# Kernel tuning notes

Hardware: AMD Instinct MI355X
Metric: run time of the kernel (lower is better)

The kernel has to match this reference:

```python
import jax, jax.numpy as jnp
import numpy as np

B, D, Q, E, H, V = 32, 1024, 64, 384, 384, 50000
PAD = 0
EPS = 1e-12


def setup_inputs() -> dict:
    key = jax.random.key(0)
    ks = jax.random.split(key, 13)
    documents = jax.random.randint(ks[0], (B, D), 1, V)
    doc_lens = jax.random.randint(ks[1], (B,), D // 2, D + 1)
    doc_valid = jnp.arange(D)[None, :] < doc_lens[:, None]
    documents = jnp.where(doc_valid, documents, PAD)
    doc_masks = doc_valid.astype(jnp.float32)[:, :, None]
    querys = jax.random.randint(ks[2], (B, Q), 1, V)
    query_lens = jax.random.randint(ks[3], (B,), Q // 2, Q + 1)
    q_valid = jnp.arange(Q)[None, :] < query_lens[:, None]
    querys = jnp.where(q_valid, querys, PAD)
    query_masks = q_valid.astype(jnp.float32)[:, :, None]
    answers = documents[:, :1]  # guaranteed present in each doc
    emb = jax.random.uniform(ks[4], (V + 1, E), jnp.float32, -0.05, 0.05)
    emb = emb.at[PAD].set(0.0)
    gw = lambda k, s: jax.random.normal(k, s, jnp.float32) * 0.05
    w_ih_f = gw(ks[5], (3 * H, E)); w_hh_f = gw(ks[6], (3 * H, H))
    b_ih_f = gw(ks[7], (3 * H,)); b_hh_f = gw(ks[8], (3 * H,))
    w_ih_b = gw(ks[9], (3 * H, E)); w_hh_b = gw(ks[10], (3 * H, H))
    b_ih_b = gw(ks[11], (3 * H,)); b_hh_b = gw(ks[12], (3 * H,))
    return dict(documents=documents, doc_lens=doc_lens, doc_masks=doc_masks,
                querys=querys, query_lens=query_lens, query_masks=query_masks,
                answers=answers, emb=emb,
                w_ih_f=w_ih_f, w_hh_f=w_hh_f, b_ih_f=b_ih_f, b_hh_f=b_hh_f,
                w_ih_b=w_ih_b, w_hh_b=w_hh_b, b_ih_b=b_ih_b, b_hh_b=b_hh_b)


def _gru_dir(x, w_ih, w_hh, b_ih, b_hh):
    # x: [B,T,E] -> outputs [B,T,H]; torch GRU cell math
    Bn = x.shape[0]
    Hn = w_hh.shape[1]
    xp = jnp.einsum('bte,ge->btg', x, w_ih) + b_ih  # precompute input projections [B,T,3H]

    def step(h, g):
        gh = h @ w_hh.T + b_hh
        i_r, i_z, i_n = jnp.split(g, 3, axis=-1)
        h_r, h_z, h_n = jnp.split(gh, 3, axis=-1)
        r = jax.nn.sigmoid(i_r + h_r)
        z = jax.nn.sigmoid(i_z + h_z)
        n = jnp.tanh(i_n + r * h_n)
        hn = (1.0 - z) * n + z * h
        return hn, hn

    h0 = jnp.zeros((Bn, Hn), x.dtype)
    _, out = jax.lax.scan(step, h0, jnp.swapaxes(xp, 0, 1))
    return jnp.swapaxes(out, 0, 1)


def _rev_within_len(x, lens):
    # reverse each sequence only over its valid prefix (emulates packed bwd GRU)
    T = x.shape[1]
    t = jnp.arange(T)
    idx = jnp.where(t[None, :] < lens[:, None], lens[:, None] - 1 - t[None, :], t[None, :])
    return jnp.take_along_axis(x, idx[:, :, None], axis=1)


def _bigru(x, lens, valid, pf, pb):
    out_f = _gru_dir(x, *pf)
    out_b = _rev_within_len(_gru_dir(_rev_within_len(x, lens), *pb), lens)
    out = jnp.concatenate([out_f, out_b], axis=-1)
    return out * valid[:, :, None]  # unpack pads with zeros


def _softmax_mask(x, mask, axis):
    shift = jnp.max(x, axis=axis, keepdims=True)
    e = jnp.exp(x - shift) * mask
    return e / (jnp.sum(e, axis=axis, keepdims=True) + EPS)


def reference(documents, doc_lens, doc_masks, querys, query_lens, query_masks, answers,
              emb, w_ih_f, w_hh_f, b_ih_f, b_hh_f, w_ih_b, w_hh_b, b_ih_b, b_hh_b):
    doc_valid = doc_masks[..., 0]
    q_valid = query_masks[..., 0]
    doc_h = _bigru(emb[documents], doc_lens, doc_valid,
                   (w_ih_f, w_hh_f, b_ih_f, b_hh_f), (w_ih_b, w_hh_b, b_ih_b, b_hh_b))
    q_h = _bigru(emb[querys], query_lens, q_valid,
                 (w_ih_f, w_hh_f, b_ih_f, b_hh_f), (w_ih_b, w_hh_b, b_ih_b, b_hh_b))
    scores = jnp.einsum('bdh,bqh->bdq', doc_h, q_h)          # IndiATT_output
    pair_mask = jnp.einsum('bdo,bqo->bdq', doc_masks, query_masks)
    alpha = _softmax_mask(scores, pair_mask, axis=1)
    beta = _softmax_mask(scores, pair_mask, axis=2)
    beta_aver = jnp.sum(beta, axis=1) / doc_lens[:, None].astype(scores.dtype)  # [B,Q]
    s = jnp.einsum('bdq,bq->bd', alpha, beta_aver)            # AoA_output squeezed
    probs = jnp.sum(s * (documents == answers).astype(s.dtype), axis=1)

    def pick(doc, sv, vv):
        sc = jnp.zeros(V + 1, s.dtype).at[doc].add(sv * vv)   # segment-sum by word id
        cnt = jnp.zeros(V + 1, s.dtype).at[doc].add(vv)
        return jnp.argmax(jnp.where(cnt > 0, sc, -jnp.inf))

    pred_answers = jax.vmap(pick)(documents, s, doc_valid)
    return probs, pred_answers
```

## Files before the change

kernel.cpp:

```cpp
#include <hip/hip_runtime.h>
#include <hip/hip_bf16.h>
#include <stdint.h>

#define EPSV 1e-12f
#define NB 32
#define DD 1024
#define QQ 64
#define EE 384
#define HH 384
#define NW 12
#define CH 256

typedef __attribute__((ext_vector_type(4))) float f32x4;
typedef __attribute__((ext_vector_type(8))) __bf16 bf16x8;
typedef __attribute__((ext_vector_type(4))) unsigned short u16x4;
typedef __attribute__((ext_vector_type(4))) int i32x4;
typedef unsigned short u16;

static __device__ __forceinline__ u16 f2bf(float f) {
  union { float f; uint32_t u; } v; v.f = f;
  uint32_t u = v.u;
  return (u16)((u + 0x7fffu + ((u >> 16) & 1u)) >> 16);
}

static __device__ __forceinline__ f32x4 MFMA(bf16x8 a, bf16x8 b, f32x4 c) {
  return __builtin_amdgcn_mfma_f32_16x16x32_bf16(a, b, c, 0, 0, 0);
}

static __device__ __forceinline__ bf16x8 ldw8(const float* p) {
  float4 a = *(const float4*)p;
  float4 b = *(const float4*)(p + 4);
  union { u16 e[8]; bf16x8 v; } u;
  u.e[0] = f2bf(a.x); u.e[1] = f2bf(a.y); u.e[2] = f2bf(a.z); u.e[3] = f2bf(a.w);
  u.e[4] = f2bf(b.x); u.e[5] = f2bf(b.y); u.e[6] = f2bf(b.z); u.e[7] = f2bf(b.w);
  return u.v;
}

static __device__ __forceinline__ void st_short_sc(u16* p, u16 v) {
  asm volatile("global_store_short %0, %1, off sc1" :: "v"(p), "v"((uint32_t)v) : "memory");
}
static __device__ __forceinline__ void ld_b128_sc(const u16* p, i32x4& d) {
  asm volatile("global_load_dwordx4 %0, %1, off sc1" : "=v"(d) : "v"(p) : "memory");
}
static __device__ __forceinline__ void st_dword_sc(unsigned* p, unsigned v) {
  asm volatile("global_store_dword %0, %1, off sc1" :: "v"(p), "v"(v) : "memory");
}
static __device__ __forceinline__ void ld_tags(const unsigned* p, i32x4& a, i32x4& b, i32x4& c,
                                               i32x4& d, i32x4& e, i32x4& f) {
  asm volatile(
      "global_load_dwordx4 %0, %6, off sc1\n\t"
      "global_load_dwordx4 %1, %6, off offset:16 sc1\n\t"
      "global_load_dwordx4 %2, %6, off offset:32 sc1\n\t"
      "global_load_dwordx4 %3, %6, off offset:48 sc1\n\t"
      "global_load_dwordx4 %4, %6, off offset:64 sc1\n\t"
      "global_load_dwordx4 %5, %6, off offset:80 sc1\n\t"
      "s_waitcnt vmcnt(0)"
      : "=&v"(a), "=&v"(b), "=&v"(c), "=&v"(d), "=&v"(e), "=&v"(f)
      : "v"(p) : "memory");
}

__global__ __launch_bounds__(256) void k_emb(const int* __restrict__ doc, const int* __restrict__ qry,
                                             const float* __restrict__ emb, u16* __restrict__ embx) {
  int i = blockIdx.x * 256 + threadIdx.x;
  int row = i / 96, e4 = i - row * 96;
  int tok = (row < NB * DD) ? doc[row] : qry[row - NB * DD];
  float4 v = ((const float4*)(emb + (size_t)tok * EE))[e4];
  u16x4 o; o.x = f2bf(v.x); o.y = f2bf(v.y); o.z = f2bf(v.z); o.w = f2bf(v.w);
  *(u16x4*)(embx + (size_t)row * EE + e4 * 4) = o;
}

__global__ __launch_bounds__(512, 2) void k_xp(
    const u16* __restrict__ embx, const int* __restrict__ doc_lens, const int* __restrict__ q_lens,
    const float* __restrict__ w_ih_f, const float* __restrict__ b_ih_f, const float* __restrict__ b_hh_f,
    const float* __restrict__ w_ih_b, const float* __restrict__ b_ih_b, const float* __restrict__ b_hh_b,
    float* __restrict__ xpd, float* __restrict__ xpq, int cbase) {
  __shared__ int lensh[32];
  const int gx = blockIdx.x;
  int corpus, d2, jblk, tch;
  if (gx < 48) { corpus = 0; d2 = gx / 24; int rem = gx % 24; jblk = rem / 4; tch = rem % 4; }
  else { corpus = 1; int g2 = gx - 48; d2 = g2 / 6; jblk = g2 % 6; tch = 0; }
  const int T = corpus ? QQ : DD;
  const int* lens = corpus ? q_lens : doc_lens;
  const float* w_ih = d2 ? w_ih_b : w_ih_f;
  const float* b_ih = d2 ? b_ih_b : b_ih_f;
  const float* b_hh = d2 ? b_hh_b : b_hh_f;
  const u16* exb = embx + (corpus ? (size_t)NB * DD * EE : 0);
  float* xpg = corpus ? (xpq + (size_t)d2 * QQ * 36864) : (xpd + (size_t)d2 * CH * 36864);
  const int tid = threadIdx.x;
  if (tid < 32) lensh[tid] = lens[tid];
  __syncthreads();
  const int lane = tid & 63, wv = tid >> 6;
  const int wslot = wv >> 1, mt = wv & 1;
  const int col = lane & 15, khi = lane >> 4;
  const int jg = jblk * 64 + wslot * 16 + col;
  const float br = b_ih[jg] + b_hh[jg];
  const float bz = b_ih[384 + jg] + b_hh[384 + jg];
  const float bn = b_ih[768 + jg];
  bf16x8 Wr[12], Wz[12], Wn[12];
#pragma unroll
  for (int ks = 0; ks < 12; ++ks) {
    Wr[ks] = ldw8(w_ih + (size_t)jg * 384 + ks * 32 + khi * 8);
    Wz[ks] = ldw8(w_ih + (size_t)(384 + jg) * 384 + ks * 32 + khi * 8);
    Wn[ks] = ldw8(w_ih + (size_t)(768 + jg) * 384 + ks * 32 + khi * 8);
  }
  const int b_a = mt * 16 + col;
  const int lenb = lensh[b_a];
  const int bh0 = mt * 16 + khi * 4;
  for (int tt = 0; tt < 64; ++tt) {
    const int s_lc = tch * 64 + tt;
    const int s_g = corpus ? s_lc : (cbase + s_lc);
    const int trow = d2 ? ((s_g < lenb) ? (lenb - 1 - s_g) : s_g) : s_g;
    const u16* ap = exb + ((size_t)b_a * T + trow) * EE + khi * 8;
    bf16x8 A[12];
#pragma unroll
    for (int ks = 0; ks < 12; ++ks) A[ks] = *(const bf16x8*)(ap + ks * 32);
    f32x4 ar{0.f, 0.f, 0.f, 0.f}, az = ar, an = ar;
#pragma unroll
    for (int ks = 0; ks < 12; ++ks) {
      ar = MFMA(A[ks], Wr[ks], ar);
      az = MFMA(A[ks], Wz[ks], az);
      an = MFMA(A[ks], Wn[ks], an);
    }
    float* op = xpg + (size_t)s_lc * 36864 + (size_t)jg * 32 + bh0;
    f32x4 o0{ar[0] + br, ar[1] + br, ar[2] + br, ar[3] + br};
    f32x4 o1{az[0] + bz, az[1] + bz, az[2] + bz, az[3] + bz};
    f32x4 o2{an[0] + bn, an[1] + bn, an[2] + bn, an[3] + bn};
    *(f32x4*)op = o0;
    *(f32x4*)(op + 384 * 32) = o1;
    *(f32x4*)(op + 768 * 32) = o2;
  }
}

__global__ __launch_bounds__(256) void k_rec(
    const float* __restrict__ xpd, const float* __restrict__ xpq,
    const int* __restrict__ doc_lens, const int* __restrict__ q_lens,
    const float* __restrict__ w_hh_f, const float* __restrict__ b_hh_f,
    const float* __restrict__ w_hh_b, const float* __restrict__ b_hh_b,
    u16* __restrict__ doc_h, u16* __restrict__ q_h,
    u16* __restrict__ h_bc, unsigned* __restrict__ cnts, unsigned* __restrict__ tags,
    float* __restrict__ h_state, int cbase, int first) {
  __shared__ u16 wfrag[36864];
  __shared__ int lensh[32];

  const int grp = blockIdx.x / NW;
  const int wg = blockIdx.x - grp * NW;
  const int corpus = grp >> 1, dir = grp & 1;
  const int T = corpus ? QQ : DD;
  const int nst = corpus ? QQ : CH;
  const int* lens = corpus ? q_lens : doc_lens;
  const float* w_hh = dir ? w_hh_b : w_hh_f;
  const float* b_hh = dir ? b_hh_b : b_hh_f;
  u16* out = corpus ? q_h : doc_h;
  const float* xpg = corpus ? (xpq + (size_t)dir * QQ * 36864) : (xpd + (size_t)dir * CH * 36864);
  u16* hb = h_bc + (size_t)grp * (2 * NB * HH);
  unsigned* cnt = cnts + (size_t)grp * 16;
  const int tid = threadIdx.x;

  if (tid < 32) lensh[tid] = lens[tid];
  for (int idx = tid; idx < 36864; idx += 256) {
    int nt = idx / 6144;
    int rem = idx - nt * 6144;
    int ks = rem >> 9;
    int le = rem & 511;
    int lane_ = le >> 3, i = le & 7;
    int g = nt >> 1, js_ = nt & 1;
    int colw = lane_ & 15, khiw = lane_ >> 4;
    int k = ks * 32 + khiw * 8 + i;
    int rowg = g * 384 + wg * 32 + js_ * 16 + colw;
    wfrag[idx] = f2bf(w_hh[(size_t)rowg * 384 + k]);
  }
  if (first) {
    for (int idx = tid; idx < 1024; idx += 256) {
      int b = idx >> 5, jl_ = idx & 31;
      st_short_sc(hb + b * HH + wg * 32 + jl_, (u16)0);
    }
    asm volatile("s_waitcnt vmcnt(0)" ::: "memory");
  }
  __syncthreads();
  if (first) {
    if (tid == 0) {
      __hip_atomic_fetch_add(cnt, 1u, __ATOMIC_RELAXED, __HIP_MEMORY_SCOPE_AGENT);
      while (__hip_atomic_load(cnt, __ATOMIC_RELAXED, __HIP_MEMORY_SCOPE_AGENT) < (unsigned)NW)
        __builtin_amdgcn_s_sleep(1);
    }
    __syncthreads();
  }

  const int lane = tid & 63, wv = tid >> 6;
  const int mt = wv >> 1, js = wv & 1;
  const int col = lane & 15, khi = lane >> 4;
  const int jg = wg * 32 + js * 16 + col;
  const float bias_hn = b_hh[768 + jg];
  const int b_x = mt * 16 + col;
  const int bh0 = mt * 16 + khi * 4;
  int len_h[4];
#pragma unroll
  for (int r = 0; r < 4; ++r) len_h[r] = lensh[bh0 + r];
  u16* outp = out + (size_t)dir * HH + jg;
  f32x4 hprev;
#pragma unroll
  for (int r = 0; r < 4; ++r)
    hprev[r] = first ? 0.f : h_state[(size_t)grp * 12288 + (size_t)jg * 32 + (bh0 + r)];

  const unsigned* tagrow = tags + (size_t)grp * 64 + mt * 32;
  unsigned* tagp = tags + (size_t)grp * 64 + mt * 32 + (wg * 2 + js);

  auto umin2 = [](unsigned a, unsigned b) { return a < b ? a : b; };
  auto pollwait = [&](unsigned need) {
    while (true) {
      i32x4 t0, t1, t2, t3, t4, t5;
      ld_tags(tagrow, t0, t1, t2, t3, t4, t5);
      unsigned mn = 0xffffffffu;
#pragma unroll
      for (int k = 0; k < 4; ++k) {
        mn = umin2(mn, (unsigned)t0[k]); mn = umin2(mn, (unsigned)t1[k]);
        mn = umin2(mn, (unsigned)t2[k]); mn = umin2(mn, (unsigned)t3[k]);
        mn = umin2(mn, (unsigned)t4[k]); mn = umin2(mn, (unsigned)t5[k]);
      }
      if (mn >= need) break;
      __builtin_amdgcn_s_sleep(1);
    }
  };
  auto load_xp = [&](f32x4* x, int sl) {
    const float* xs = xpg + (size_t)sl * 36864;
#pragma unroll
    for (int g = 0; g < 3; ++g)
      x[g] = *(const f32x4*)(xs + ((size_t)(g * 384 + jg)) * 32 + bh0);
  };

  f32x4 xpA[3], xpB[3];
  load_xp(xpA, 0);

  auto step = [&](int sl, f32x4* xc, f32x4* xn) {
    const int s = cbase + sl;
    const int p = s & 1;
    const u16* rbuf = hb + p * (NB * HH);
    u16* wbuf = hb + (p ^ 1) * (NB * HH);
    pollwait((unsigned)s);
    i32x4 areg[12];
    const u16* ahp = rbuf + b_x * HH + khi * 8;
#pragma unroll
    for (int ks = 0; ks < 12; ++ks) ld_b128_sc(ahp + ks * 32, areg[ks]);
    asm volatile("s_waitcnt vmcnt(0)" ::: "memory");
    __builtin_amdgcn_sched_barrier(0);
    f32x4 acc_r{0.f, 0.f, 0.f, 0.f};
    f32x4 acc_z = acc_r, acc_nh = acc_r;
#pragma unroll
    for (int ks = 0; ks < 12; ++ks) {
      bf16x8 af = __builtin_bit_cast(bf16x8, areg[ks]);
      bf16x8 br = *(const bf16x8*)&wfrag[((js) * 12 + ks) * 512 + lane * 8];
      bf16x8 bz = *(const bf16x8*)&wfrag[((2 + js) * 12 + ks) * 512 + lane * 8];
      bf16x8 bn = *(const bf16x8*)&wfrag[((4 + js) * 12 + ks) * 512 + lane * 8];
      acc_r = MFMA(af, br, acc_r);
      acc_z = MFMA(af, bz, acc_z);
      acc_nh = MFMA(af, bn, acc_nh);
    }
    u16 hq[4];
#pragma unroll
    for (int r = 0; r < 4; ++r) {
      const int b = bh0 + r;
      float rg = 1.f / (1.f + __expf(-(acc_r[r] + xc[0][r])));
      float zg = 1.f / (1.f + __expf(-(acc_z[r] + xc[1][r])));
      float ng = tanhf(xc[2][r] + rg * (acc_nh[r] + bias_hn));
      float hn = (1.f - zg) * ng + zg * hprev[r];
      hprev[r] = hn;
      hq[r] = f2bf(hn);
      st_short_sc(wbuf + b * HH + jg, hq[r]);
    }
    asm volatile("s_waitcnt vmcnt(0)" ::: "memory");
    if (lane == 0) st_dword_sc(tagp, (unsigned)(s + 1));
    load_xp(xn, (sl + 1 < nst) ? (sl + 1) : sl);
#pragma unroll
    for (int r = 0; r < 4; ++r) {
      const int b = bh0 + r;
      const int len = len_h[r];
      const int tro = dir ? ((s < len) ? (len - 1 - s) : s) : s;
      outp[((size_t)b * T + tro) * (2 * HH)] = hq[r];
    }
  };

  for (int sl = 0; sl < nst; sl += 2) {
    step(sl, xpA, xpB);
    step(sl + 1, xpB, xpA);
  }
#pragma unroll
  for (int r = 0; r < 4; ++r)
    h_state[(size_t)grp * 12288 + (size_t)jg * 32 + (bh0 + r)] = hprev[r];
}

__global__ __launch_bounds__(256) void k_scores(
    const u16* __restrict__ doc_h, const u16* __restrict__ q_h,
    const int* __restrict__ doc_lens, const int* __restrict__ q_lens,
    float* __restrict__ SM, float* __restrict__ rowmax, float* __restrict__ rowsum) {
  const int b = blockIdx.x >> 4, dblk = blockIdx.x & 15;
  const int tid = threadIdx.x, lane = tid & 63, wv = tid >> 6;
  const int col = lane & 15, khi = lane >> 4;
  const int dlen = doc_lens[b], qlen = q_lens[b];
  const u16* dp = doc_h + ((size_t)(b * DD + dblk * 64 + wv * 16 + col)) * (2 * HH) + khi * 8;
  const u16* qp = q_h + (size_t)b * QQ * (2 * HH);
  f32x4 acc[4];
#pragma unroll
  for (int nt = 0; nt < 4; ++nt) acc[nt] = f32x4{0.f, 0.f, 0.f, 0.f};
  for (int ks = 0; ks < 24; ++ks) {
    bf16x8 av = *(const bf16x8*)(dp + ks * 32);
#pragma unroll
    for (int nt = 0; nt < 4; ++nt) {
      bf16x8 bv = *(const bf16x8*)(qp + (size_t)(nt * 16 + col) * (2 * HH) + ks * 32 + khi * 8);
      acc[nt] = MFMA(av, bv, acc[nt]);
    }
  }
  const int d0 = dblk * 64 + wv * 16 + khi * 4;
  float* smb = SM + (size_t)b * DD * QQ;
#pragma unroll
  for (int r = 0; r < 4; ++r) {
    const int d = d0 + r;
    const bool dv = d < dlen;
    float v[4];
#pragma unroll
    for (int nt = 0; nt < 4; ++nt) {
      const int q = nt * 16 + col;
      v[nt] = (dv && q < qlen) ? acc[nt][r] : 0.f;
      smb[(size_t)d * QQ + q] = v[nt];
    }
    float mx = fmaxf(fmaxf(v[0], v[1]), fmaxf(v[2], v[3]));
#pragma unroll
    for (int off = 1; off < 16; off <<= 1) mx = fmaxf(mx, __shfl_xor(mx, off, 64));
    float sm = 0.f;
#pragma unroll
    for (int nt = 0; nt < 4; ++nt) {
      const int q = nt * 16 + col;
      if (dv && q < qlen) sm += __expf(v[nt] - mx);
    }
#pragma unroll
    for (int off = 1; off < 16; off <<= 1) sm += __shfl_xor(sm, off, 64);
    if (col == 0) { rowmax[b * DD + d] = mx; rowsum[b * DD + d] = sm; }
  }
}

__global__ __launch_bounds__(256) void k_cols(
    const float* __restrict__ SM, const float* __restrict__ rowmax, const float* __restrict__ rowsum,
    const int* __restrict__ doc_lens, const int* __restrict__ q_lens,
    float* __restrict__ colmax, float* __restrict__ colsum, float* __restrict__ bav) {
  const int b = blockIdx.x, tid = threadIdx.x;
  const int q = tid & 63, dg = tid >> 6;
  __shared__ float red[4][64];
  __shared__ float cmx[64];
  const float* smb = SM + (size_t)b * DD * QQ;
  float cm = -3.0e38f;
  for (int d = dg; d < DD; d += 4) cm = fmaxf(cm, smb[(size_t)d * QQ + q]);
  red[dg][q] = cm;
  __syncthreads();
  if (tid < 64) cmx[tid] = fmaxf(fmaxf(red[0][tid], red[1][tid]), fmaxf(red[2][tid], red[3][tid]));
  __syncthreads();
  const int dlen = doc_lens[b];
  const bool qv = q < q_lens[b];
  const float cmq = cmx[q];
  float cs = 0.f, ba = 0.f;
  for (int d = dg; d < DD; d += 4) {
    if (qv && d < dlen) {
      float v = smb[(size_t)d * QQ + q];
      cs += __expf(v - cmq);
      ba += __expf(v - rowmax[b * DD + d]) / (rowsum[b * DD + d] + EPSV);
    }
  }
  __syncthreads();
  red[dg][q] = cs;
  __syncthreads();
  float cst = 0.f;
  if (tid < 64) cst = red[0][tid] + red[1][tid] + red[2][tid] + red[3][tid];
  __syncthreads();
  red[dg][q] = ba;
  __syncthreads();
  if (tid < 64) {
    float bat = red[0][tid] + red[1][tid] + red[2][tid] + red[3][tid];
    colmax[b * QQ + tid] = cmx[tid];
    colsum[b * QQ + tid] = cst;
    bav[b * QQ + tid] = bat / (float)dlen;
  }
}

__global__ __launch_bounds__(256) void k_s(
    const float* __restrict__ SM, const float* __restrict__ colmax, const float* __restrict__ colsum,
    const float* __restrict__ bav, const int* __restrict__ doc_lens, const int* __restrict__ q_lens,
    const int* __restrict__ documents, const int* __restrict__ answers,
    float* __restrict__ sc, float* __restrict__ cnt_tok, float* __restrict__ dout) {
  const int b = blockIdx.x >> 2, dblk = blockIdx.x & 3;
  const int tid = threadIdx.x;
  __shared__ float cm[64], cs[64], bv[64];
  __shared__ int qm[64];
  if (tid < 64) {
    cm[tid] = colmax[b * QQ + tid];
    cs[tid] = colsum[b * QQ + tid];
    bv[tid] = bav[b * QQ + tid];
    qm[tid] = (tid < q_lens[b]) ? 1 : 0;
  }
  __syncthreads();
  const int d = dblk * 256 + tid;
  const bool dv = d < doc_lens[b];
  const float* smr = SM + ((size_t)b * DD + d) * QQ;
  float sd = 0.f;
#pragma unroll
  for (int q = 0; q < 64; ++q) {
    float e = (dv && qm[q]) ? __expf(smr[q] - cm[q]) : 0.f;
    sd += e / (cs[q] + EPSV) * bv[q];
  }
  const int tok = documents[b * DD + d];
  if (tok == answers[b]) atomicAdd(&dout[b], sd);
  if (dv) {
    atomicAdd(&sc[(size_t)b * 50001 + tok], sd);
    atomicAdd(&cnt_tok[(size_t)b * 50001 + tok], 1.0f);
  }
}

__global__ __launch_bounds__(256) void k_pred(
    const float* __restrict__ sc, const float* __restrict__ cnt_tok, float* __restrict__ dout) {
  const int b = blockIdx.x, tid = threadIdx.x;
  __shared__ float bvs[256];
  __shared__ int bis[256];
  float bvv = -3.0e38f;
  int bii = 0x7fffffff;
  for (int i = tid; i < 50001; i += 256) {
    if (cnt_tok[(size_t)b * 50001 + i] > 0.f) {
      float v = sc[(size_t)b * 50001 + i];
      if (v > bvv) { bvv = v; bii = i; }
    }
  }
  bvs[tid] = bvv;
  bis[tid] = bii;
  __syncthreads();
  for (int st = 128; st > 0; st >>= 1) {
    if (tid < st) {
      float v2 = bvs[tid + st];
      int i2 = bis[tid + st];
      if (v2 > bvs[tid] || (v2 == bvs[tid] && i2 < bis[tid])) { bvs[tid] = v2; bis[tid] = i2; }
    }
    __syncthreads();
  }
  if (tid == 0) dout[32 + b] = (float)bis[0];
}

extern "C" void kernel_launch(void* const* d_in, const int* in_sizes, int n_in,
                              void* d_out, int out_size, void* d_ws, size_t ws_size,
                              hipStream_t stream) {
  const int* documents = (const int*)d_in[0];
  const int* doc_lens = (const int*)d_in[1];
  const int* querys = (const int*)d_in[3];
  const int* query_lens = (const int*)d_in[4];
  const int* answers = (const int*)d_in[6];
  const float* emb = (const float*)d_in[7];
  const float* w_ih_f = (const float*)d_in[8];
  const float* w_hh_f = (const float*)d_in[9];
  const float* b_ih_f = (const float*)d_in[10];
  const float* b_hh_f = (const float*)d_in[11];
  const float* w_ih_b = (const float*)d_in[12];
  const float* w_hh_b = (const float*)d_in[13];
  const float* b_ih_b = (const float*)d_in[14];
  const float* b_hh_b = (const float*)d_in[15];
  float* dout = (float*)d_out;
  char* ws = (char*)d_ws;

  size_t o = 0;
  auto alloc = [&](size_t bytes) { size_t r = o; o += (bytes + 255) & ~(size_t)255; return r; };
  size_t o_embx = alloc((size_t)34816 * 384 * 2);
  size_t o_xpd  = alloc((size_t)2 * CH * 36864 * 4);
  size_t o_xpq  = alloc((size_t)2 * QQ * 36864 * 4);
  size_t o_doch = alloc((size_t)NB * DD * 768 * 2);
  size_t o_qh   = alloc((size_t)NB * QQ * 768 * 2);
  size_t o_hbc  = alloc((size_t)4 * 2 * NB * HH * 2);
  size_t o_hst  = alloc((size_t)4 * HH * NB * 4);
  size_t o_cnt  = alloc((size_t)4 * 16 * 4);
  size_t o_tag  = alloc((size_t)4 * 64 * 4);
  size_t o_sync_end = o;
  size_t o_SM   = alloc((size_t)NB * DD * QQ * 4);
  size_t o_rmax = alloc((size_t)NB * DD * 4);
  size_t o_rsum = alloc((size_t)NB * DD * 4);
  size_t o_cmax = alloc((size_t)NB * QQ * 4);
  size_t o_csum = alloc((size_t)NB * QQ * 4);
  size_t o_bav  = alloc((size_t)NB * QQ * 4);
  size_t o_sc   = alloc((size_t)NB * 50001 * 4);
  size_t o_ctk  = alloc((size_t)NB * 50001 * 4);
  (void)ws_size; (void)in_sizes; (void)n_in; (void)out_size;

  hipMemsetAsync(ws + o_cnt, 0, o_sync_end - o_cnt, stream);
  hipMemsetAsync(ws + o_sc, 0, (o_ctk - o_sc) + (size_t)NB * 50001 * 4, stream);
  hipMemsetAsync(d_out, 0, 64 * sizeof(float), stream);

  k_emb<<<13056, 256, 0, stream>>>(documents, querys, emb, (u16*)(ws + o_embx));
  for (int c = 0; c < 4; ++c) {
    const int cbase = c * CH;
    k_xp<<<c == 0 ? 60 : 48, 512, 0, stream>>>(
        (u16*)(ws + o_embx), doc_lens, query_lens,
        w_ih_f, b_ih_f, b_hh_f, w_ih_b, b_ih_b, b_hh_b,
        (float*)(ws + o_xpd), (float*)(ws + o_xpq), cbase);
    k_rec<<<c == 0 ? 48 : 24, 256, 0, stream>>>(
        (float*)(ws + o_xpd), (float*)(ws + o_xpq), doc_lens, query_lens,
        w_hh_f, b_hh_f, w_hh_b, b_hh_b,
        (u16*)(ws + o_doch), (u16*)(ws + o_qh),
        (u16*)(ws + o_hbc), (unsigned*)(ws + o_cnt), (unsigned*)(ws + o_tag),
        (float*)(ws + o_hst), cbase, c == 0 ? 1 : 0);
  }
  k_scores<<<512, 256, 0, stream>>>((u16*)(ws + o_doch), (u16*)(ws + o_qh), doc_lens, query_lens,
                                    (float*)(ws + o_SM), (float*)(ws + o_rmax), (float*)(ws + o_rsum));
  k_cols<<<32, 256, 0, stream>>>((float*)(ws + o_SM), (float*)(ws + o_rmax), (float*)(ws + o_rsum),
                                 doc_lens, query_lens,
                                 (float*)(ws + o_cmax), (float*)(ws + o_csum), (float*)(ws + o_bav));
  k_s<<<128, 256, 0, stream>>>((float*)(ws + o_SM), (float*)(ws + o_cmax), (float*)(ws + o_csum),
                               (float*)(ws + o_bav), doc_lens, query_lens, documents, answers,
                               (float*)(ws + o_sc), (float*)(ws + o_ctk), dout);
  k_pred<<<32, 256, 0, stream>>>((float*)(ws + o_sc), (float*)(ws + o_ctk), dout);
}
```

Before: 5.779 ms.

## Add service wavefront in recurrence kernel to prefetch xp and scatter outputs

Adds a fifth wavefront to each recurrence workgroup that prefetches the input-projection slices into a 4-deep LDS ring and takes over the strided global writes of hidden outputs, staged through an LDS buffer. The four compute wavefronts now only poll for the hidden state, run the MFMAs, publish h and signal through LDS flags. The goal is to take xp load latency and scattered output stores off the serial per-step critical path. In exchange it adds LDS flag polling and more LDS use, and it risks stalls if the service wave falls behind.

```diff
diff --git a/kernel.cpp b/kernel.cpp
--- a/kernel.cpp
+++ b/kernel.cpp
@@ -131,7 +131,7 @@
   }
 }
 
-__global__ __launch_bounds__(256) void k_rec(
+__global__ __launch_bounds__(320, 1) void k_rec(
     const float* __restrict__ xpd, const float* __restrict__ xpq,
     const int* __restrict__ doc_lens, const int* __restrict__ q_lens,
     const float* __restrict__ w_hh_f, const float* __restrict__ b_hh_f,
@@ -140,7 +140,12 @@
     u16* __restrict__ h_bc, unsigned* __restrict__ cnts, unsigned* __restrict__ tags,
     float* __restrict__ h_state, int cbase, int first) {
   __shared__ u16 wfrag[36864];
+  __shared__ float xp_l[4 * 3072];
+  __shared__ u16 out_l[4 * 1024];
   __shared__ int lensh[32];
+  __shared__ unsigned xp_rdy[4];
+  __shared__ unsigned out_rdy[4];
+  __shared__ unsigned svc_done;
 
   const int grp = blockIdx.x / NW;
   const int wg = blockIdx.x - grp * NW;
@@ -155,9 +160,12 @@
   u16* hb = h_bc + (size_t)grp * (2 * NB * HH);
   unsigned* cnt = cnts + (size_t)grp * 16;
   const int tid = threadIdx.x;
+  const int wv = tid >> 6, lane = tid & 63;
 
   if (tid < 32) lensh[tid] = lens[tid];
-  for (int idx = tid; idx < 36864; idx += 256) {
+  if (tid < 4) { xp_rdy[tid] = 0; out_rdy[tid] = 0; }
+  if (tid == 8) svc_done = 0;
+  for (int idx = tid; idx < 36864; idx += 320) {
     int nt = idx / 6144;
     int rem = idx - nt * 6144;
     int ks = rem >> 9;
@@ -170,7 +178,7 @@
     wfrag[idx] = f2bf(w_hh[(size_t)rowg * 384 + k]);
   }
   if (first) {
-    for (int idx = tid; idx < 1024; idx += 256) {
+    for (int idx = tid; idx < 1024; idx += 320) {
       int b = idx >> 5, jl_ = idx & 31;
       st_short_sc(hb + b * HH + wg * 32 + jl_, (u16)0);
     }
@@ -186,106 +194,144 @@
     __syncthreads();
   }
 
-  const int lane = tid & 63, wv = tid >> 6;
-  const int mt = wv >> 1, js = wv & 1;
-  const int col = lane & 15, khi = lane >> 4;
-  const int jg = wg * 32 + js * 16 + col;
-  const float bias_hn = b_hh[768 + jg];
-  const int b_x = mt * 16 + col;
-  const int bh0 = mt * 16 + khi * 4;
-  int len_h[4];
-#pragma unroll
-  for (int r = 0; r < 4; ++r) len_h[r] = lensh[bh0 + r];
-  u16* outp = out + (size_t)dir * HH + jg;
-  f32x4 hprev;
-#pragma unroll
-  for (int r = 0; r < 4; ++r)
-    hprev[r] = first ? 0.f : h_state[(size_t)grp * 12288 + (size_t)jg * 32 + (bh0 + r)];
-
-  const unsigned* tagrow = tags + (size_t)grp * 64 + mt * 32;
-  unsigned* tagp = tags + (size_t)grp * 64 + mt * 32 + (wg * 2 + js);
-
-  auto umin2 = [](unsigned a, unsigned b) { return a < b ? a : b; };
-  auto pollwait = [&](unsigned need) {
-    while (true) {
-      i32x4 t0, t1, t2, t3, t4, t5;
-      ld_tags(tagrow, t0, t1, t2, t3, t4, t5);
-      unsigned mn = 0xffffffffu;
-#pragma unroll
-      for (int k = 0; k < 4; ++k) {
-        mn = umin2(mn, (unsigned)t0[k]); mn = umin2(mn, (unsigned)t1[k]);
-        mn = umin2(mn, (unsigned)t2[k]); mn = umin2(mn, (unsigned)t3[k]);
-        mn = umin2(mn, (unsigned)t4[k]); mn = umin2(mn, (unsigned)t5[k]);
+  auto lds_wait_ge = [&](unsigned* f, unsigned need) {
+    while (__hip_atomic_load(f, __ATOMIC_RELAXED, __HIP_MEMORY_SCOPE_WORKGROUP) < need)
+      __builtin_amdgcn_s_sleep(1);
+  };
+  auto lds_post = [&](unsigned* f, unsigned v) {
+    asm volatile("s_waitcnt lgkmcnt(0)" ::: "memory");
+    __hip_atomic_store(f, v, __ATOMIC_RELAXED, __HIP_MEMORY_SCOPE_WORKGROUP);
+  };
+
+  if (wv == 4) {
+    auto svc_load_xp = [&](int k) {
+      const int slot = k & 3;
+      const float* src = xpg + (size_t)k * 36864 + (size_t)(wg * 32) * 32;
+      f32x4 v0[4], v1[4], v2[4];
+#pragma unroll
+      for (int i = 0; i < 4; ++i) v0[i] = *(const f32x4*)(src + lane * 16 + i * 4);
+#pragma unroll
+      for (int i = 0; i < 4; ++i) v1[i] = *(const f32x4*)(src + 384 * 32 + lane * 16 + i * 4);
+#pragma unroll
+      for (int i = 0; i < 4; ++i) v2[i] = *(const f32x4*)(src + 768 * 32 + lane * 16 + i * 4);
+#pragma unroll
+      for (int i = 0; i < 4; ++i) *(f32x4*)&xp_l[slot * 3072 + lane * 16 + i * 4] = v0[i];
+#pragma unroll
+      for (int i = 0; i < 4; ++i) *(f32x4*)&xp_l[slot * 3072 + 1024 + lane * 16 + i * 4] = v1[i];
+#pragma unroll
+      for (int i = 0; i < 4; ++i) *(f32x4*)&xp_l[slot * 3072 + 2048 + lane * 16 + i * 4] = v2[i];
+      if (lane == 0) lds_post(&xp_rdy[slot], (unsigned)(k + 1));
+    };
+    for (int k = 0; k < 3 && k < nst; ++k) svc_load_xp(k);
+    const int d0 = lane >> 1;
+    const int bh = (lane & 1) * 16;
+    u16* outps = out + (size_t)dir * HH + (wg * 32 + d0);
+    for (int sl = 0; sl < nst; ++sl) {
+#pragma unroll
+      for (int w = 0; w < 4; ++w) lds_wait_ge(&out_rdy[w], (unsigned)(sl + 1));
+      const int slot = sl & 3;
+      union { i32x4 v; u16 e[8]; } o0, o1;
+      o0.v = *(i32x4*)&out_l[slot * 1024 + d0 * 32 + bh];
+      o1.v = *(i32x4*)&out_l[slot * 1024 + d0 * 32 + bh + 8];
+      const int s = cbase + sl;
+#pragma unroll
+      for (int r = 0; r < 16; ++r) {
+        const int b = bh + r;
+        const u16 hv = (r < 8) ? o0.e[r] : o1.e[r - 8];
+        const int len = lensh[b];
+        const int tro = dir ? ((s < len) ? (len - 1 - s) : s) : s;
+        outps[((size_t)b * T + tro) * (2 * HH)] = hv;
       }
-      if (mn >= need) break;
-      __builtin_amdgcn_s_sleep(1);
-    }
-  };
-  auto load_xp = [&](f32x4* x, int sl) {
-    const float* xs = xpg + (size_t)sl * 36864;
-#pragma unroll
-    for (int g = 0; g < 3; ++g)
-      x[g] = *(const f32x4*)(xs + ((size_t)(g * 384 + jg)) * 32 + bh0);
-  };
-
-  f32x4 xpA[3], xpB[3];
-  load_xp(xpA, 0);
-
-  auto step = [&](int sl, f32x4* xc, f32x4* xn) {
-    const int s = cbase + sl;
-    const int p = s & 1;
-    const u16* rbuf = hb + p * (NB * HH);
-    u16* wbuf = hb + (p ^ 1) * (NB * HH);
-    pollwait((unsigned)s);
-    i32x4 areg[12];
-    const u16* ahp = rbuf + b_x * HH + khi * 8;
-#pragma unroll
-    for (int ks = 0; ks < 12; ++ks) ld_b128_sc(ahp + ks * 32, areg[ks]);
-    asm volatile("s_waitcnt vmcnt(0)" ::: "memory");
-    __builtin_amdgcn_sched_barrier(0);
-    f32x4 acc_r{0.f, 0.f, 0.f, 0.f};
-    f32x4 acc_z = acc_r, acc_nh = acc_r;
-#pragma unroll
-    for (int ks = 0; ks < 12; ++ks) {
-      bf16x8 af = __builtin_bit_cast(bf16x8, areg[ks]);
-      bf16x8 br = *(const bf16x8*)&wfrag[((js) * 12 + ks) * 512 + lane * 8];
-      bf16x8 bz = *(const bf16x8*)&wfrag[((2 + js) * 12 + ks) * 512 + lane * 8];
-      bf16x8 bn = *(const bf16x8*)&wfrag[((4 + js) * 12 + ks) * 512 + lane * 8];
-      acc_r = MFMA(af, br, acc_r);
-      acc_z = MFMA(af, bz, acc_z);
-      acc_nh = MFMA(af, bn, acc_nh);
-    }
-    u16 hq[4];
-#pragma unroll
-    for (int r = 0; r < 4; ++r) {
-      const int b = bh0 + r;
-      float rg = 1.f / (1.f + __expf(-(acc_r[r] + xc[0][r])));
-      float zg = 1.f / (1.f + __expf(-(acc_z[r] + xc[1][r])));
-      float ng = tanhf(xc[2][r] + rg * (acc_nh[r] + bias_hn));
-      float hn = (1.f - zg) * ng + zg * hprev[r];
-      hprev[r] = hn;
-      hq[r] = f2bf(hn);
-      st_short_sc(wbuf + b * HH + jg, hq[r]);
-    }
-    asm volatile("s_waitcnt vmcnt(0)" ::: "memory");
-    if (lane == 0) st_dword_sc(tagp, (unsigned)(s + 1));
-    load_xp(xn, (sl + 1 < nst) ? (sl + 1) : sl);
-#pragma unroll
-    for (int r = 0; r < 4; ++r) {
-      const int b = bh0 + r;
-      const int len = len_h[r];
-      const int tro = dir ? ((s < len) ? (len - 1 - s) : s) : s;
-      outp[((size_t)b * T + tro) * (2 * HH)] = hq[r];
-    }
-  };
-
-  for (int sl = 0; sl < nst; sl += 2) {
-    step(sl, xpA, xpB);
-    step(sl + 1, xpB, xpA);
-  }
-#pragma unroll
-  for (int r = 0; r < 4; ++r)
-    h_state[(size_t)grp * 12288 + (size_t)jg * 32 + (bh0 + r)] = hprev[r];
+      if (lane == 0) lds_post(&svc_done, (unsigned)(sl + 1));
+      if (sl + 3 < nst) svc_load_xp(sl + 3);
+    }
+  } else {
+    const int mt = wv >> 1, js = wv & 1;
+    const int col = lane & 15, khi = lane >> 4;
+    const int jg = wg * 32 + js * 16 + col;
+    const int dml = js * 16 + col;
+    const float bias_hn = b_hh[768 + jg];
+    const int b_x = mt * 16 + col;
+    const int bh0 = mt * 16 + khi * 4;
+    f32x4 hprev;
+#pragma unroll
+    for (int r = 0; r < 4; ++r)
+      hprev[r] = first ? 0.f : h_state[(size_t)grp * 12288 + (size_t)jg * 32 + (bh0 + r)];
+
+    const unsigned* tagrow = tags + (size_t)grp * 64 + mt * 32;
+    unsigned* tagp = tags + (size_t)grp * 64 + mt * 32 + (wg * 2 + js);
+    auto umin2 = [](unsigned a, unsigned b) { return a < b ? a : b; };
+    auto pollwait = [&](unsigned need) {
+      while (true) {
+        i32x4 t0, t1, t2, t3, t4, t5;
+        ld_tags(tagrow, t0, t1, t2, t3, t4, t5);
+        unsigned mn = 0xffffffffu;
+#pragma unroll
+        for (int k = 0; k < 4; ++k) {
+          mn = umin2(mn, (unsigned)t0[k]); mn = umin2(mn, (unsigned)t1[k]);
+          mn = umin2(mn, (unsigned)t2[k]); mn = umin2(mn, (unsigned)t3[k]);
+          mn = umin2(mn, (unsigned)t4[k]); mn = umin2(mn, (unsigned)t5[k]);
+        }
+        if (mn >= need) break;
+        __builtin_amdgcn_s_sleep(1);
+      }
+    };
+
+    for (int sl = 0; sl < nst; ++sl) {
+      const int s = cbase + sl;
+      const int p = s & 1;
+      const u16* rbuf = hb + p * (NB * HH);
+      u16* wbuf = hb + (p ^ 1) * (NB * HH);
+      pollwait((unsigned)s);
+      i32x4 areg[12];
+      const u16* ahp = rbuf + b_x * HH + khi * 8;
+#pragma unroll
+      for (int ks = 0; ks < 12; ++ks) ld_b128_sc(ahp + ks * 32, areg[ks]);
+      asm volatile("s_waitcnt vmcnt(0)" ::: "memory");
+      __builtin_amdgcn_sched_barrier(0);
+      lds_wait_ge(&xp_rdy[sl & 3], (unsigned)(sl + 1));
+      const float* xb = &xp_l[(sl & 3) * 3072 + dml * 32 + bh0];
+      f32x4 x0 = *(const f32x4*)(xb);
+      f32x4 x1 = *(const f32x4*)(xb + 1024);
+      f32x4 x2 = *(const f32x4*)(xb + 2048);
+      f32x4 acc_r{0.f, 0.f, 0.f, 0.f};
+      f32x4 acc_z = acc_r, acc_nh = acc_r;
+#pragma unroll
+      for (int ks = 0; ks < 12; ++ks) {
+        bf16x8 af = __builtin_bit_cast(bf16x8, areg[ks]);
+        bf16x8 br = *(const bf16x8*)&wfrag[((js) * 12 + ks) * 512 + lane * 8];
+        bf16x8 bz = *(const bf16x8*)&wfrag[((2 + js) * 12 + ks) * 512 + lane * 8];
+        bf16x8 bn = *(const bf16x8*)&wfrag[((4 + js) * 12 + ks) * 512 + lane * 8];
+        acc_r = MFMA(af, br, acc_r);
+        acc_z = MFMA(af, bz, acc_z);
+        acc_nh = MFMA(af, bn, acc_nh);
+      }
+      u16 hq[4];
+#pragma unroll
+      for (int r = 0; r < 4; ++r) {
+        const int b = bh0 + r;
+        float rg = 1.f / (1.f + __expf(-(acc_r[r] + x0[r])));
+        float zg = 1.f / (1.f + __expf(-(acc_z[r] + x1[r])));
+        float ng = tanhf(x2[r] + rg * (acc_nh[r] + bias_hn));
+        float hn = (1.f - zg) * ng + zg * hprev[r];
+        hprev[r] = hn;
+        hq[r] = f2bf(hn);
+        st_short_sc(wbuf + b * HH + jg, hq[r]);
+      }
+      if (sl >= 4) lds_wait_ge(&svc_done, (unsigned)(sl - 3));
+      uint2 pk;
+      pk.x = (uint32_t)hq[0] | ((uint32_t)hq[1] << 16);
+      pk.y = (uint32_t)hq[2] | ((uint32_t)hq[3] << 16);
+      *(uint2*)&out_l[(sl & 3) * 1024 + dml * 32 + bh0] = pk;
+      asm volatile("s_waitcnt vmcnt(0)" ::: "memory");
+      if (lane == 0) st_dword_sc(tagp, (unsigned)(s + 1));
+      if (lane == 0) lds_post(&out_rdy[wv], (unsigned)(sl + 1));
+      else asm volatile("s_waitcnt lgkmcnt(0)" ::: "memory");
+    }
+#pragma unroll
+    for (int r = 0; r < 4; ++r)
+      h_state[(size_t)grp * 12288 + (size_t)jg * 32 + (bh0 + r)] = hprev[r];
+  }
 }
 
 __global__ __launch_bounds__(256) void k_scores(
@@ -492,7 +538,7 @@
         (u16*)(ws + o_embx), doc_lens, query_lens,
         w_ih_f, b_ih_f, b_hh_f, w_ih_b, b_ih_b, b_hh_b,
         (float*)(ws + o_xpd), (float*)(ws + o_xpq), cbase);
-    k_rec<<<c == 0 ? 48 : 24, 256, 0, stream>>>(
+    k_rec<<<c == 0 ? 48 : 24, 320, 0, stream>>>(
         (float*)(ws + o_xpd), (float*)(ws + o_xpq), doc_lens, query_lens,
         w_hh_f, b_hh_f, w_hh_b, b_hh_b,
         (u16*)(ws + o_doch), (u16*)(ws + o_qh),
```

Measured after the change: 6.290 ms. +8.8%, slower.

## Replace tag-counter barrier with sentinel-polled per-step hidden-state history

Applied to the files above, without the earlier changes.

The recurrent kernel no longer publishes per-wave step tags and polls them before reading the double-buffered hidden state. Each step now writes h into its own slot of a buffer that holds every timestep, pre-filled with 0xFF. Consumers spin-load the h slice directly until no 0xFFFF sentinel halfwords remain. This removes the store-drain, tag store and separate tag poll from each step's critical path, so a cross-workgroup handoff costs one round trip instead of two. In exchange it adds a roughly 100 MB memset per call and assumes a real bf16 hidden value is never exactly 0xFFFF.

```diff
diff --git a/kernel.cpp b/kernel.cpp
--- a/kernel.cpp
+++ b/kernel.cpp
@@ -39,23 +39,25 @@
 static __device__ __forceinline__ void st_short_sc(u16* p, u16 v) {
   asm volatile("global_store_short %0, %1, off sc1" :: "v"(p), "v"((uint32_t)v) : "memory");
 }
-static __device__ __forceinline__ void ld_b128_sc(const u16* p, i32x4& d) {
-  asm volatile("global_load_dwordx4 %0, %1, off sc1" : "=v"(d) : "v"(p) : "memory");
-}
-static __device__ __forceinline__ void st_dword_sc(unsigned* p, unsigned v) {
-  asm volatile("global_store_dword %0, %1, off sc1" :: "v"(p), "v"(v) : "memory");
-}
-static __device__ __forceinline__ void ld_tags(const unsigned* p, i32x4& a, i32x4& b, i32x4& c,
-                                               i32x4& d, i32x4& e, i32x4& f) {
+static __device__ __forceinline__ void ld_h12(const u16* p,
+    i32x4& d0, i32x4& d1, i32x4& d2, i32x4& d3, i32x4& d4, i32x4& d5,
+    i32x4& d6, i32x4& d7, i32x4& d8, i32x4& d9, i32x4& d10, i32x4& d11) {
   asm volatile(
-      "global_load_dwordx4 %0, %6, off sc1\n\t"
-      "global_load_dwordx4 %1, %6, off offset:16 sc1\n\t"
-      "global_load_dwordx4 %2, %6, off offset:32 sc1\n\t"
-      "global_load_dwordx4 %3, %6, off offset:48 sc1\n\t"
-      "global_load_dwordx4 %4, %6, off offset:64 sc1\n\t"
-      "global_load_dwordx4 %5, %6, off offset:80 sc1\n\t"
+      "global_load_dwordx4 %0, %12, off sc1\n\t"
+      "global_load_dwordx4 %1, %12, off offset:64 sc1\n\t"
+      "global_load_dwordx4 %2, %12, off offset:128 sc1\n\t"
+      "global_load_dwordx4 %3, %12, off offset:192 sc1\n\t"
+      "global_load_dwordx4 %4, %12, off offset:256 sc1\n\t"
+      "global_load_dwordx4 %5, %12, off offset:320 sc1\n\t"
+      "global_load_dwordx4 %6, %12, off offset:384 sc1\n\t"
+      "global_load_dwordx4 %7, %12, off offset:448 sc1\n\t"
+      "global_load_dwordx4 %8, %12, off offset:512 sc1\n\t"
+      "global_load_dwordx4 %9, %12, off offset:576 sc1\n\t"
+      "global_load_dwordx4 %10, %12, off offset:640 sc1\n\t"
+      "global_load_dwordx4 %11, %12, off offset:704 sc1\n\t"
       "s_waitcnt vmcnt(0)"
-      : "=&v"(a), "=&v"(b), "=&v"(c), "=&v"(d), "=&v"(e), "=&v"(f)
+      : "=&v"(d0), "=&v"(d1), "=&v"(d2), "=&v"(d3), "=&v"(d4), "=&v"(d5),
+        "=&v"(d6), "=&v"(d7), "=&v"(d8), "=&v"(d9), "=&v"(d10), "=&v"(d11)
       : "v"(p) : "memory");
 }
 
@@ -137,8 +139,7 @@
     const float* __restrict__ w_hh_f, const float* __restrict__ b_hh_f,
     const float* __restrict__ w_hh_b, const float* __restrict__ b_hh_b,
     u16* __restrict__ doc_h, u16* __restrict__ q_h,
-    u16* __restrict__ h_bc, unsigned* __restrict__ cnts, unsigned* __restrict__ tags,
-    float* __restrict__ h_state, int cbase, int first) {
+    u16* __restrict__ h_all, float* __restrict__ h_state, int cbase, int first) {
   __shared__ u16 wfrag[36864];
   __shared__ int lensh[32];
 
@@ -152,8 +153,7 @@
   const float* b_hh = dir ? b_hh_b : b_hh_f;
   u16* out = corpus ? q_h : doc_h;
   const float* xpg = corpus ? (xpq + (size_t)dir * QQ * 36864) : (xpd + (size_t)dir * CH * 36864);
-  u16* hb = h_bc + (size_t)grp * (2 * NB * HH);
-  unsigned* cnt = cnts + (size_t)grp * 16;
+  u16* ha = h_all + (size_t)grp * ((DD + 1) * NB * HH);
   const int tid = threadIdx.x;
 
   if (tid < 32) lensh[tid] = lens[tid];
@@ -165,26 +165,18 @@
     int lane_ = le >> 3, i = le & 7;
     int g = nt >> 1, js_ = nt & 1;
     int colw = lane_ & 15, khiw = lane_ >> 4;
-    int k = ks * 32 + khiw * 8 + i;
+    int k = ks * 32 + (lane_ >> 4) * 8 + i;
     int rowg = g * 384 + wg * 32 + js_ * 16 + colw;
+    (void)khiw;
     wfrag[idx] = f2bf(w_hh[(size_t)rowg * 384 + k]);
   }
   if (first) {
     for (int idx = tid; idx < 1024; idx += 256) {
       int b = idx >> 5, jl_ = idx & 31;
-      st_short_sc(hb + b * HH + wg * 32 + jl_, (u16)0);
-    }
-    asm volatile("s_waitcnt vmcnt(0)" ::: "memory");
-  }
-  __syncthreads();
-  if (first) {
-    if (tid == 0) {
-      __hip_atomic_fetch_add(cnt, 1u, __ATOMIC_RELAXED, __HIP_MEMORY_SCOPE_AGENT);
-      while (__hip_atomic_load(cnt, __ATOMIC_RELAXED, __HIP_MEMORY_SCOPE_AGENT) < (unsigned)NW)
-        __builtin_amdgcn_s_sleep(1);
-    }
-    __syncthreads();
-  }
+      st_short_sc(ha + (size_t)b * HH + wg * 32 + jl_, (u16)0);
+    }
+  }
+  __syncthreads();
 
   const int lane = tid & 63, wv = tid >> 6;
   const int mt = wv >> 1, js = wv & 1;
@@ -202,25 +194,6 @@
   for (int r = 0; r < 4; ++r)
     hprev[r] = first ? 0.f : h_state[(size_t)grp * 12288 + (size_t)jg * 32 + (bh0 + r)];
 
-  const unsigned* tagrow = tags + (size_t)grp * 64 + mt * 32;
-  unsigned* tagp = tags + (size_t)grp * 64 + mt * 32 + (wg * 2 + js);
-
-  auto umin2 = [](unsigned a, unsigned b) { return a < b ? a : b; };
-  auto pollwait = [&](unsigned need) {
-    while (true) {
-      i32x4 t0, t1, t2, t3, t4, t5;
-      ld_tags(tagrow, t0, t1, t2, t3, t4, t5);
-      unsigned mn = 0xffffffffu;
-#pragma unroll
-      for (int k = 0; k < 4; ++k) {
-        mn = umin2(mn, (unsigned)t0[k]); mn = umin2(mn, (unsigned)t1[k]);
-        mn = umin2(mn, (unsigned)t2[k]); mn = umin2(mn, (unsigned)t3[k]);
-        mn = umin2(mn, (unsigned)t4[k]); mn = umin2(mn, (unsigned)t5[k]);
-      }
-      if (mn >= need) break;
-      __builtin_amdgcn_s_sleep(1);
-    }
-  };
   auto load_xp = [&](f32x4* x, int sl) {
     const float* xs = xpg + (size_t)sl * 36864;
 #pragma unroll
@@ -233,16 +206,26 @@
 
   auto step = [&](int sl, f32x4* xc, f32x4* xn) {
     const int s = cbase + sl;
-    const int p = s & 1;
-    const u16* rbuf = hb + p * (NB * HH);
-    u16* wbuf = hb + (p ^ 1) * (NB * HH);
-    pollwait((unsigned)s);
-    i32x4 areg[12];
-    const u16* ahp = rbuf + b_x * HH + khi * 8;
-#pragma unroll
-    for (int ks = 0; ks < 12; ++ks) ld_b128_sc(ahp + ks * 32, areg[ks]);
-    asm volatile("s_waitcnt vmcnt(0)" ::: "memory");
+    const u16* ahp = ha + (size_t)s * (NB * HH) + (size_t)b_x * HH + khi * 8;
+    i32x4 a0, a1, a2, a3, a4, a5, a6, a7, a8, a9, a10, a11;
+    while (true) {
+      ld_h12(ahp, a0, a1, a2, a3, a4, a5, a6, a7, a8, a9, a10, a11);
+      uint32_t bad = 0;
+      auto chk = [&](const i32x4& d) {
+#pragma unroll
+        for (int k = 0; k < 4; ++k) {
+          uint32_t u = (uint32_t)d[k];
+          bad |= ((u & 0xFFFFu) == 0xFFFFu);
+          bad |= ((u >> 16) == 0xFFFFu);
+        }
+      };
+      chk(a0); chk(a1); chk(a2); chk(a3); chk(a4); chk(a5);
+      chk(a6); chk(a7); chk(a8); chk(a9); chk(a10); chk(a11);
+      if (__all(bad == 0)) break;
+      __builtin_amdgcn_s_sleep(1);
+    }
     __builtin_amdgcn_sched_barrier(0);
+    i32x4 areg[12] = {a0, a1, a2, a3, a4, a5, a6, a7, a8, a9, a10, a11};
     f32x4 acc_r{0.f, 0.f, 0.f, 0.f};
     f32x4 acc_z = acc_r, acc_nh = acc_r;
 #pragma unroll
@@ -256,6 +239,7 @@
       acc_nh = MFMA(af, bn, acc_nh);
     }
     u16 hq[4];
+    u16* wslice = ha + (size_t)(s + 1) * (NB * HH);
 #pragma unroll
     for (int r = 0; r < 4; ++r) {
       const int b = bh0 + r;
@@ -265,10 +249,8 @@
       float hn = (1.f - zg) * ng + zg * hprev[r];
       hprev[r] = hn;
       hq[r] = f2bf(hn);
-      st_short_sc(wbuf + b * HH + jg, hq[r]);
-    }
-    asm volatile("s_waitcnt vmcnt(0)" ::: "memory");
-    if (lane == 0) st_dword_sc(tagp, (unsigned)(s + 1));
+      st_short_sc(wslice + (size_t)b * HH + jg, hq[r]);
+    }
     load_xp(xn, (sl + 1 < nst) ? (sl + 1) : sl);
 #pragma unroll
     for (int r = 0; r < 4; ++r) {
@@ -464,13 +446,10 @@
   size_t o_embx = alloc((size_t)34816 * 384 * 2);
   size_t o_xpd  = alloc((size_t)2 * CH * 36864 * 4);
   size_t o_xpq  = alloc((size_t)2 * QQ * 36864 * 4);
+  size_t o_hall = alloc((size_t)4 * (DD + 1) * NB * HH * 2);
   size_t o_doch = alloc((size_t)NB * DD * 768 * 2);
   size_t o_qh   = alloc((size_t)NB * QQ * 768 * 2);
-  size_t o_hbc  = alloc((size_t)4 * 2 * NB * HH * 2);
   size_t o_hst  = alloc((size_t)4 * HH * NB * 4);
-  size_t o_cnt  = alloc((size_t)4 * 16 * 4);
-  size_t o_tag  = alloc((size_t)4 * 64 * 4);
-  size_t o_sync_end = o;
   size_t o_SM   = alloc((size_t)NB * DD * QQ * 4);
   size_t o_rmax = alloc((size_t)NB * DD * 4);
   size_t o_rsum = alloc((size_t)NB * DD * 4);
@@ -481,7 +460,7 @@
   size_t o_ctk  = alloc((size_t)NB * 50001 * 4);
   (void)ws_size; (void)in_sizes; (void)n_in; (void)out_size;
 
-  hipMemsetAsync(ws + o_cnt, 0, o_sync_end - o_cnt, stream);
+  hipMemsetAsync(ws + o_hall, 0xFF, (size_t)4 * (DD + 1) * NB * HH * 2, stream);
   hipMemsetAsync(ws + o_sc, 0, (o_ctk - o_sc) + (size_t)NB * 50001 * 4, stream);
   hipMemsetAsync(d_out, 0, 64 * sizeof(float), stream);
 
@@ -496,8 +475,7 @@
         (float*)(ws + o_xpd), (float*)(ws + o_xpq), doc_lens, query_lens,
         w_hh_f, b_hh_f, w_hh_b, b_hh_b,
         (u16*)(ws + o_doch), (u16*)(ws + o_qh),
-        (u16*)(ws + o_hbc), (unsigned*)(ws + o_cnt), (unsigned*)(ws + o_tag),
-        (float*)(ws + o_hst), cbase, c == 0 ? 1 : 0);
+        (u16*)(ws + o_hall), (float*)(ws + o_hst), cbase, c == 0 ? 1 : 0);
   }
   k_scores<<<512, 256, 0, stream>>>((u16*)(ws + o_doch), (u16*)(ws + o_qh), doc_lens, query_lens,
                                     (float*)(ws + o_SM), (float*)(ws + o_rmax), (float*)(ws + o_rsum));
```

After: 6.339 ms. 1.1x slower.

## Overlap next-chunk input projection with GRU recurrence using double-buffered xp

Applied to the files above, without the earlier changes.

The per-chunk k_xp launch before each recurrence is removed. Extra blocks appended to the k_rec grid now compute the input projections for the next document chunk into a second xp buffer while the recurrence blocks consume the current one. This hides the projection GEMM behind the latency-bound recurrence and drops three kernel launches, at the cost of doubling the xp workspace. The extra blocks share the device with the spin-synchronised recurrence blocks and may contend with them for memory bandwidth.

```diff
diff --git a/kernel.cpp b/kernel.cpp
--- a/kernel.cpp
+++ b/kernel.cpp
@@ -10,6 +10,7 @@
 #define HH 384
 #define NW 12
 #define CH 256
+#define XPBUF ((size_t)2 * CH * 36864)
 
 typedef __attribute__((ext_vector_type(4))) float f32x4;
 typedef __attribute__((ext_vector_type(8))) __bf16 bf16x8;
@@ -132,18 +133,79 @@
 }
 
 __global__ __launch_bounds__(256) void k_rec(
-    const float* __restrict__ xpd, const float* __restrict__ xpq,
+    const float* __restrict__ xp_rd, float* __restrict__ xp_wr, const float* __restrict__ xpq,
     const int* __restrict__ doc_lens, const int* __restrict__ q_lens,
     const float* __restrict__ w_hh_f, const float* __restrict__ b_hh_f,
     const float* __restrict__ w_hh_b, const float* __restrict__ b_hh_b,
     u16* __restrict__ doc_h, u16* __restrict__ q_h,
     u16* __restrict__ h_bc, unsigned* __restrict__ cnts, unsigned* __restrict__ tags,
-    float* __restrict__ h_state, int cbase, int first) {
+    float* __restrict__ h_state,
+    const u16* __restrict__ embx,
+    const float* __restrict__ w_ih_f, const float* __restrict__ b_ih_f,
+    const float* __restrict__ w_ih_b, const float* __restrict__ b_ih_b,
+    int cbase, int first, int rec_blocks) {
   __shared__ u16 wfrag[36864];
   __shared__ int lensh[32];
-
-  const int grp = blockIdx.x / NW;
-  const int wg = blockIdx.x - grp * NW;
+  const int bid = blockIdx.x;
+  const int tid = threadIdx.x;
+
+  if (bid >= rec_blocks) {
+    const int e = bid - rec_blocks;
+    const int d2 = e / 48;
+    const int rem = e - d2 * 48;
+    const int jb = rem >> 2, tch = rem & 3;
+    const float* w_ih = d2 ? w_ih_b : w_ih_f;
+    const float* b_ih = d2 ? b_ih_b : b_ih_f;
+    const float* b_hh2 = d2 ? b_hh_b : b_hh_f;
+    float* xpo = xp_wr + (size_t)d2 * CH * 36864;
+    if (tid < 32) lensh[tid] = doc_lens[tid];
+    __syncthreads();
+    const int lane = tid & 63, wv = tid >> 6;
+    const int wslot = wv >> 1, mt = wv & 1;
+    const int col = lane & 15, khi = lane >> 4;
+    const int jg = jb * 32 + wslot * 16 + col;
+    const float br = b_ih[jg] + b_hh2[jg];
+    const float bz = b_ih[384 + jg] + b_hh2[384 + jg];
+    const float bn = b_ih[768 + jg];
+    bf16x8 Wr[12], Wz[12], Wn[12];
+#pragma unroll
+    for (int ks = 0; ks < 12; ++ks) {
+      Wr[ks] = ldw8(w_ih + (size_t)jg * 384 + ks * 32 + khi * 8);
+      Wz[ks] = ldw8(w_ih + (size_t)(384 + jg) * 384 + ks * 32 + khi * 8);
+      Wn[ks] = ldw8(w_ih + (size_t)(768 + jg) * 384 + ks * 32 + khi * 8);
+    }
+    const int b_a = mt * 16 + col;
+    const int lenb = lensh[b_a];
+    const int bh0 = mt * 16 + khi * 4;
+    const int cb2 = cbase + CH;
+    for (int tt = 0; tt < 64; ++tt) {
+      const int s_lc = tch * 64 + tt;
+      const int s_g = cb2 + s_lc;
+      const int trow = d2 ? ((s_g < lenb) ? (lenb - 1 - s_g) : s_g) : s_g;
+      const u16* ap = embx + ((size_t)b_a * DD + trow) * EE + khi * 8;
+      bf16x8 A[12];
+#pragma unroll
+      for (int ks = 0; ks < 12; ++ks) A[ks] = *(const bf16x8*)(ap + ks * 32);
+      f32x4 ar{0.f, 0.f, 0.f, 0.f}, az = ar, an = ar;
+#pragma unroll
+      for (int ks = 0; ks < 12; ++ks) {
+        ar = MFMA(A[ks], Wr[ks], ar);
+        az = MFMA(A[ks], Wz[ks], az);
+        an = MFMA(A[ks], Wn[ks], an);
+      }
+      float* op = xpo + (size_t)s_lc * 36864 + (size_t)jg * 32 + bh0;
+      f32x4 o0{ar[0] + br, ar[1] + br, ar[2] + br, ar[3] + br};
+      f32x4 o1{az[0] + bz, az[1] + bz, az[2] + bz, az[3] + bz};
+      f32x4 o2{an[0] + bn, an[1] + bn, an[2] + bn, an[3] + bn};
+      *(f32x4*)op = o0;
+      *(f32x4*)(op + 384 * 32) = o1;
+      *(f32x4*)(op + 768 * 32) = o2;
+    }
+    return;
+  }
+
+  const int grp = bid / NW;
+  const int wg = bid - grp * NW;
   const int corpus = grp >> 1, dir = grp & 1;
   const int T = corpus ? QQ : DD;
   const int nst = corpus ? QQ : CH;
@@ -151,10 +213,9 @@
   const float* w_hh = dir ? w_hh_b : w_hh_f;
   const float* b_hh = dir ? b_hh_b : b_hh_f;
   u16* out = corpus ? q_h : doc_h;
-  const float* xpg = corpus ? (xpq + (size_t)dir * QQ * 36864) : (xpd + (size_t)dir * CH * 36864);
+  const float* xpg = corpus ? (xpq + (size_t)dir * QQ * 36864) : (xp_rd + (size_t)dir * CH * 36864);
   u16* hb = h_bc + (size_t)grp * (2 * NB * HH);
   unsigned* cnt = cnts + (size_t)grp * 16;
-  const int tid = threadIdx.x;
 
   if (tid < 32) lensh[tid] = lens[tid];
   for (int idx = tid; idx < 36864; idx += 256) {
@@ -164,8 +225,8 @@
     int le = rem & 511;
     int lane_ = le >> 3, i = le & 7;
     int g = nt >> 1, js_ = nt & 1;
-    int colw = lane_ & 15, khiw = lane_ >> 4;
-    int k = ks * 32 + khiw * 8 + i;
+    int colw = lane_ & 15;
+    int k = ks * 32 + (lane_ >> 4) * 8 + i;
     int rowg = g * 384 + wg * 32 + js_ * 16 + colw;
     wfrag[idx] = f2bf(w_hh[(size_t)rowg * 384 + k]);
   }
@@ -462,7 +523,7 @@
   size_t o = 0;
   auto alloc = [&](size_t bytes) { size_t r = o; o += (bytes + 255) & ~(size_t)255; return r; };
   size_t o_embx = alloc((size_t)34816 * 384 * 2);
-  size_t o_xpd  = alloc((size_t)2 * CH * 36864 * 4);
+  size_t o_xpd  = alloc((size_t)2 * XPBUF * 4);
   size_t o_xpq  = alloc((size_t)2 * QQ * 36864 * 4);
   size_t o_doch = alloc((size_t)NB * DD * 768 * 2);
   size_t o_qh   = alloc((size_t)NB * QQ * 768 * 2);
@@ -486,18 +547,22 @@
   hipMemsetAsync(d_out, 0, 64 * sizeof(float), stream);
 
   k_emb<<<13056, 256, 0, stream>>>(documents, querys, emb, (u16*)(ws + o_embx));
+  k_xp<<<60, 512, 0, stream>>>((u16*)(ws + o_embx), doc_lens, query_lens,
+                               w_ih_f, b_ih_f, b_hh_f, w_ih_b, b_ih_b, b_hh_b,
+                               (float*)(ws + o_xpd), (float*)(ws + o_xpq), 0);
   for (int c = 0; c < 4; ++c) {
-    const int cbase = c * CH;
-    k_xp<<<c == 0 ? 60 : 48, 512, 0, stream>>>(
-        (u16*)(ws + o_embx), doc_lens, query_lens,
-        w_ih_f, b_ih_f, b_hh_f, w_ih_b, b_ih_b, b_hh_b,
-        (float*)(ws + o_xpd), (float*)(ws + o_xpq), cbase);
-    k_rec<<<c == 0 ? 48 : 24, 256, 0, stream>>>(
-        (float*)(ws + o_xpd), (float*)(ws + o_xpq), doc_lens, query_lens,
+    const int rec_blocks = (c == 0) ? 48 : 24;
+    const int xp_blocks = (c < 3) ? 96 : 0;
+    float* xp_rd = (float*)(ws + o_xpd) + (size_t)(c & 1) * XPBUF;
+    float* xp_wr = (float*)(ws + o_xpd) + (size_t)((c + 1) & 1) * XPBUF;
+    k_rec<<<rec_blocks + xp_blocks, 256, 0, stream>>>(
+        xp_rd, xp_wr, (float*)(ws + o_xpq), doc_lens, query_lens,
         w_hh_f, b_hh_f, w_hh_b, b_hh_b,
         (u16*)(ws + o_doch), (u16*)(ws + o_qh),
         (u16*)(ws + o_hbc), (unsigned*)(ws + o_cnt), (unsigned*)(ws + o_tag),
-        (float*)(ws + o_hst), cbase, c == 0 ? 1 : 0);
+        (float*)(ws + o_hst),
+        (u16*)(ws + o_embx), w_ih_f, b_ih_f, w_ih_b, b_ih_b,
+        c * CH, c == 0 ? 1 : 0, rec_blocks);
   }
   k_scores<<<512, 256, 0, stream>>>((u16*)(ws + o_doch), (u16*)(ws + o_qh), doc_lens, query_lens,
                                     (float*)(ws + o_SM), (float*)(ws + o_rmax), (float*)(ws + o_rsum));
```

After: 5.285 ms, median of 2. -8.5%, faster.
